# Performance work log

Hardware: AMD Instinct MI355X
Metric: run time of the kernel (lower is better)

The kernel has to match this reference:

```python
import jax, jax.numpy as jnp
import numpy as np

# Module config (from init_kwargs): causal=False, window_size=(256,256), window_type=0,
# softmax_scale=None -> 1/sqrt(D), dropout=0 (eval mode).
WINDOW_LEFT, WINDOW_RIGHT = 256, 256


def _window_mask(Sq, Sk, causal, use_window_mask):
    """Boolean [Sq, Sk] visibility mask, FA2 semantics (right-aligned offset)."""
    qi = jnp.arange(Sq)[:, None]
    kj = jnp.arange(Sk)[None, :]
    offset = Sk - Sq
    if causal:
        return kj <= qi + offset  # window (-1, 0)
    if use_window_mask:
        m = jnp.ones((Sq, Sk), dtype=bool)
        if WINDOW_LEFT >= 0:
            m = m & (kj >= qi + offset - WINDOW_LEFT)
        if WINDOW_RIGHT >= 0:
            m = m & (kj <= qi + offset + WINDOW_RIGHT)
        return m
    return None  # full attention


def setup_inputs() -> dict:
    key = jax.random.key(0)
    kq, kkv = jax.random.split(key)
    B, Sq, Sk, H, D = 2, 2048, 2048, 16, 64
    q = jax.random.normal(kq, (B, Sq, H, D), dtype=jnp.float32)
    kv = jax.random.normal(kkv, (B, Sk, 2, H, D), dtype=jnp.float32)
    return {"q": q, "kv": kv, "causal": 0, "use_window_mask": 1, "return_attn_probs": 0}


def reference(q, kv, causal, use_window_mask, return_attn_probs):
    # q: (B, Sq, H, D); kv: (B, Sk, 2, H, D)
    B, Sq, H, D = q.shape
    Sk = kv.shape[1]
    k = kv[:, :, 0]  # (B, Sk, H, D)
    v = kv[:, :, 1]
    scale = 1.0 / (D ** 0.5)
    scores = jnp.einsum('bqhd,bkhd->bhqk', q, k) * scale  # (B, H, Sq, Sk)
    mask = _window_mask(Sq, Sk, bool(causal), bool(use_window_mask))
    if mask is not None:
        scores = jnp.where(mask[None, None], scores, jnp.finfo(scores.dtype).min)
    probs = jax.nn.softmax(scores, axis=-1)
    out = jnp.einsum('bhqk,bkhd->bqhd', probs, v)  # (B, Sq, H, D)
    return out
```

## Files before the change

### kernel.cpp

```cpp
#include <hip/hip_runtime.h>
#include <hip/hip_bf16.h>

#define B_    2
#define SQ_   2048
#define SK_   2048
#define NH_   16
#define DH_   64
#define WIN_  256
#define NEG_  -30000.0f

typedef __bf16 bf16_t;
typedef bf16_t bf16x8 __attribute__((ext_vector_type(8)));
typedef bf16_t bf16x4 __attribute__((ext_vector_type(4)));
typedef float  f32x4  __attribute__((ext_vector_type(4)));

#define KSTRIDE 72
#define VSTRIDE 40
#define PSTRIDE 40

__global__ __launch_bounds__(256, 2)
void fa_fwd(const float* __restrict__ qg, const float* __restrict__ kvg,
            float* __restrict__ outg) {
  const int tid  = threadIdx.x;
  const int wid  = tid >> 6;
  const int lane = tid & 63;
  const int quad = lane >> 4;
  const int li   = lane & 15;

  const int bid = blockIdx.x;
  const int qb  = bid & 31;
  const int bh  = bid >> 5;
  const int b   = bh >> 4;
  const int h   = bh & 15;

  const int q0b = qb * 64;
  const int q0  = q0b + wid * 16;

  __shared__ __align__(16) bf16_t sK [32 * KSTRIDE];
  __shared__ __align__(16) bf16_t sVT[64 * VSTRIDE];
  __shared__ __align__(16) bf16_t sP [4 * 16 * PSTRIDE];
  bf16_t* pl = sP + wid * 16 * PSTRIDE;

  const float qscale = 0.125f * 1.44269504088896340736f;
  const float* qrow = qg + ((size_t)((b * SQ_ + q0 + li) * NH_ + h)) * DH_;
  bf16x8 qfrag[2];
#pragma unroll
  for (int c = 0; c < 2; ++c) {
    f32x4 a0 = *(const f32x4*)(qrow + c * 32 + quad * 8);
    f32x4 a1 = *(const f32x4*)(qrow + c * 32 + quad * 8 + 4);
#pragma unroll
    for (int i = 0; i < 4; ++i) {
      qfrag[c][i]     = (bf16_t)(a0[i] * qscale);
      qfrag[c][i + 4] = (bf16_t)(a1[i] * qscale);
    }
  }

  f32x4 oacc[4];
#pragma unroll
  for (int t = 0; t < 4; ++t) { f32x4 z = {0.f, 0.f, 0.f, 0.f}; oacc[t] = z; }
  float m = NEG_, l = 0.f;

  int klo = q0b - WIN_; if (klo < 0) klo = 0; klo &= ~31;
  int khi = q0b + 63 + WIN_ + 1; if (khi > SK_) khi = SK_; khi = (khi + 31) & ~31;

  const float* kbase = kvg + (size_t)b * SK_ * 2 * NH_ * DH_ + (size_t)h * DH_;
  const float* vbase = kbase + NH_ * DH_;
  const size_t krow_stride = 2 * NH_ * DH_;

  const int skey = tid >> 3;
  const int sd0  = (tid & 7) * 8;

  for (int kk = klo; kk < khi; kk += 32) {
    {
      const float* kr = kbase + (size_t)(kk + skey) * krow_stride + sd0;
      f32x4 a0 = *(const f32x4*)kr;
      f32x4 a1 = *(const f32x4*)(kr + 4);
      bf16x8 w;
#pragma unroll
      for (int i = 0; i < 4; ++i) { w[i] = (bf16_t)a0[i]; w[i + 4] = (bf16_t)a1[i]; }
      *(bf16x8*)(sK + skey * KSTRIDE + sd0) = w;

      const float* vr = vbase + (size_t)(kk + skey) * krow_stride + sd0;
      f32x4 b0 = *(const f32x4*)vr;
      f32x4 b1 = *(const f32x4*)(vr + 4);
#pragma unroll
      for (int i = 0; i < 4; ++i) {
        sVT[(sd0 + i)     * VSTRIDE + skey] = (bf16_t)b0[i];
        sVT[(sd0 + 4 + i) * VSTRIDE + skey] = (bf16_t)b1[i];
      }
    }
    __syncthreads();

    f32x4 sc[2];
#pragma unroll
    for (int s = 0; s < 2; ++s) {
      bf16x8 kf0 = *(const bf16x8*)(sK + (s * 16 + li) * KSTRIDE + quad * 8);
      bf16x8 kf1 = *(const bf16x8*)(sK + (s * 16 + li) * KSTRIDE + 32 + quad * 8);
      f32x4 acc = {0.f, 0.f, 0.f, 0.f};
      acc = __builtin_amdgcn_mfma_f32_16x16x32_bf16(kf0, qfrag[0], acc, 0, 0, 0);
      acc = __builtin_amdgcn_mfma_f32_16x16x32_bf16(kf1, qfrag[1], acc, 0, 0, 0);
      sc[s] = acc;
    }

    const int qa = q0 + li;
#pragma unroll
    for (int s = 0; s < 2; ++s)
#pragma unroll
      for (int r = 0; r < 4; ++r) {
        int key = kk + s * 16 + quad * 4 + r;
        unsigned dd = (unsigned)(key - qa + WIN_);
        if (dd > 2u * WIN_) sc[s][r] = NEG_;
      }

    float tmax = fmaxf(fmaxf(fmaxf(sc[0][0], sc[0][1]), fmaxf(sc[0][2], sc[0][3])),
                       fmaxf(fmaxf(sc[1][0], sc[1][1]), fmaxf(sc[1][2], sc[1][3])));
    tmax = fmaxf(tmax, __shfl_xor(tmax, 16));
    tmax = fmaxf(tmax, __shfl_xor(tmax, 32));
    float mnew  = fmaxf(m, tmax);
    float alpha = exp2f(m - mnew);
    float psum = 0.f;
    bf16x4 pk[2];
#pragma unroll
    for (int s = 0; s < 2; ++s)
#pragma unroll
      for (int r = 0; r < 4; ++r) {
        float p = exp2f(sc[s][r] - mnew);
        psum += p;
        pk[s][r] = (bf16_t)p;
      }
    psum += __shfl_xor(psum, 16);
    psum += __shfl_xor(psum, 32);
    l = l * alpha + psum;
    m = mnew;

#pragma unroll
    for (int s = 0; s < 2; ++s)
      *(bf16x4*)(pl + li * PSTRIDE + s * 16 + quad * 4) = pk[s];

    __syncthreads();

    float al[4];
#pragma unroll
    for (int r = 0; r < 4; ++r) al[r] = __shfl(alpha, quad * 4 + r);
#pragma unroll
    for (int t = 0; t < 4; ++t) {
      oacc[t][0] *= al[0]; oacc[t][1] *= al[1];
      oacc[t][2] *= al[2]; oacc[t][3] *= al[3];
    }

    bf16x8 pf = *(const bf16x8*)(pl + li * PSTRIDE + quad * 8);
#pragma unroll
    for (int t = 0; t < 4; ++t) {
      bf16x8 vf = *(const bf16x8*)(sVT + (16 * t + li) * VSTRIDE + quad * 8);
      oacc[t] = __builtin_amdgcn_mfma_f32_16x16x32_bf16(pf, vf, oacc[t], 0, 0, 0);
    }
    __syncthreads();
  }

  float rl[4];
#pragma unroll
  for (int r = 0; r < 4; ++r) {
    float lv = __shfl(l, quad * 4 + r);
    rl[r] = 1.0f / lv;
  }
  float* orow = outg + ((size_t)((b * SQ_ + q0) * NH_ + h)) * DH_;
#pragma unroll
  for (int t = 0; t < 4; ++t)
#pragma unroll
    for (int r = 0; r < 4; ++r)
      orow[(size_t)(quad * 4 + r) * (NH_ * DH_) + 16 * t + li] = oacc[t][r] * rl[r];
}

extern "C" void kernel_launch(void* const* d_in, const int* in_sizes, int n_in,
                              void* d_out, int out_size, void* d_ws, size_t ws_size,
                              hipStream_t stream) {
  (void)in_sizes; (void)n_in; (void)out_size; (void)d_ws; (void)ws_size;
  const float* q  = (const float*)d_in[0];
  const float* kv = (const float*)d_in[1];
  float* out = (float*)d_out;
  dim3 grid(B_ * NH_ * (SQ_ / 64));
  fa_fwd<<<grid, 256, 0, stream>>>(q, kv, out);
}
```

Before: 133.8 us.

## Enlarge query and key tiles, prefetch KV into registers, drop mid-iteration barrier

Each block now handles 128 queries, with each wave owning two 16-row query tiles, and processes 64 keys per step, so every K/V tile staged in shared memory is reused by twice as many queries. The next K/V chunk is loaded into registers while the current chunk is computed, and the barrier between writing P and reading it is replaced with an LDS waitcnt, since each wave only reads its own P rows. Block indexing is reordered so that heads vary fastest. The cost is higher register pressure and fewer blocks (512 instead of 1024), which may reduce occupancy and the number of waves available to hide latency.

```diff
diff --git a/kernel.cpp b/kernel.cpp
--- a/kernel.cpp
+++ b/kernel.cpp
@@ -15,8 +15,8 @@
 typedef float  f32x4  __attribute__((ext_vector_type(4)));
 
 #define KSTRIDE 72
-#define VSTRIDE 40
-#define PSTRIDE 40
+#define VSTRIDE 72
+#define PSTRIDE 72
 
 __global__ __launch_bounds__(256, 2)
 void fa_fwd(const float* __restrict__ qg, const float* __restrict__ kvg,
@@ -28,147 +28,182 @@
   const int li   = lane & 15;
 
   const int bid = blockIdx.x;
-  const int qb  = bid & 31;
-  const int bh  = bid >> 5;
+  const int qb  = bid >> 5;
+  const int bh  = bid & 31;
   const int b   = bh >> 4;
   const int h   = bh & 15;
 
-  const int q0b = qb * 64;
-  const int q0  = q0b + wid * 16;
-
-  __shared__ __align__(16) bf16_t sK [32 * KSTRIDE];
+  const int q0b = qb * 128;
+  const int q0  = q0b + wid * 32;
+
+  __shared__ __align__(16) bf16_t sK [64 * KSTRIDE];
   __shared__ __align__(16) bf16_t sVT[64 * VSTRIDE];
-  __shared__ __align__(16) bf16_t sP [4 * 16 * PSTRIDE];
-  bf16_t* pl = sP + wid * 16 * PSTRIDE;
+  __shared__ __align__(16) bf16_t sP [4 * 32 * PSTRIDE];
+  bf16_t* pl = sP + wid * 32 * PSTRIDE;
 
   const float qscale = 0.125f * 1.44269504088896340736f;
-  const float* qrow = qg + ((size_t)((b * SQ_ + q0 + li) * NH_ + h)) * DH_;
-  bf16x8 qfrag[2];
-#pragma unroll
-  for (int c = 0; c < 2; ++c) {
-    f32x4 a0 = *(const f32x4*)(qrow + c * 32 + quad * 8);
-    f32x4 a1 = *(const f32x4*)(qrow + c * 32 + quad * 8 + 4);
-#pragma unroll
-    for (int i = 0; i < 4; ++i) {
-      qfrag[c][i]     = (bf16_t)(a0[i] * qscale);
-      qfrag[c][i + 4] = (bf16_t)(a1[i] * qscale);
-    }
-  }
-
-  f32x4 oacc[4];
-#pragma unroll
-  for (int t = 0; t < 4; ++t) { f32x4 z = {0.f, 0.f, 0.f, 0.f}; oacc[t] = z; }
-  float m = NEG_, l = 0.f;
-
-  int klo = q0b - WIN_; if (klo < 0) klo = 0; klo &= ~31;
-  int khi = q0b + 63 + WIN_ + 1; if (khi > SK_) khi = SK_; khi = (khi + 31) & ~31;
+  bf16x8 qfrag[2][2];
+#pragma unroll
+  for (int qt = 0; qt < 2; ++qt) {
+    const float* qrow = qg + ((size_t)((b * SQ_ + q0 + qt * 16 + li) * NH_ + h)) * DH_;
+#pragma unroll
+    for (int c = 0; c < 2; ++c) {
+      f32x4 a0 = *(const f32x4*)(qrow + c * 32 + quad * 8);
+      f32x4 a1 = *(const f32x4*)(qrow + c * 32 + quad * 8 + 4);
+#pragma unroll
+      for (int i = 0; i < 4; ++i) {
+        qfrag[qt][c][i]     = (bf16_t)(a0[i] * qscale);
+        qfrag[qt][c][i + 4] = (bf16_t)(a1[i] * qscale);
+      }
+    }
+  }
+
+  f32x4 oacc[2][4];
+#pragma unroll
+  for (int qt = 0; qt < 2; ++qt)
+#pragma unroll
+    for (int t = 0; t < 4; ++t) { f32x4 z = {0.f, 0.f, 0.f, 0.f}; oacc[qt][t] = z; }
+  float m[2] = {NEG_, NEG_}, l[2] = {0.f, 0.f};
+
+  int klo = q0b - WIN_; if (klo < 0) klo = 0;
+  int khi = q0b + 127 + WIN_ + 1; if (khi > SK_) khi = SK_;
 
   const float* kbase = kvg + (size_t)b * SK_ * 2 * NH_ * DH_ + (size_t)h * DH_;
   const float* vbase = kbase + NH_ * DH_;
   const size_t krow_stride = 2 * NH_ * DH_;
 
-  const int skey = tid >> 3;
-  const int sd0  = (tid & 7) * 8;
-
-  for (int kk = klo; kk < khi; kk += 32) {
+  const int skey = tid >> 2;
+  const int sd0  = (tid & 3) * 16;
+
+  f32x4 ka[4], va[4];
+  {
+    const float* kr = kbase + (size_t)(klo + skey) * krow_stride + sd0;
+    const float* vr = vbase + (size_t)(klo + skey) * krow_stride + sd0;
+#pragma unroll
+    for (int i = 0; i < 4; ++i) { ka[i] = *(const f32x4*)(kr + 4 * i); va[i] = *(const f32x4*)(vr + 4 * i); }
+  }
+
+  for (int kk = klo; kk < khi; kk += 64) {
     {
-      const float* kr = kbase + (size_t)(kk + skey) * krow_stride + sd0;
-      f32x4 a0 = *(const f32x4*)kr;
-      f32x4 a1 = *(const f32x4*)(kr + 4);
-      bf16x8 w;
-#pragma unroll
-      for (int i = 0; i < 4; ++i) { w[i] = (bf16_t)a0[i]; w[i + 4] = (bf16_t)a1[i]; }
-      *(bf16x8*)(sK + skey * KSTRIDE + sd0) = w;
-
-      const float* vr = vbase + (size_t)(kk + skey) * krow_stride + sd0;
-      f32x4 b0 = *(const f32x4*)vr;
-      f32x4 b1 = *(const f32x4*)(vr + 4);
+      bf16x8 w0, w1;
 #pragma unroll
       for (int i = 0; i < 4; ++i) {
-        sVT[(sd0 + i)     * VSTRIDE + skey] = (bf16_t)b0[i];
-        sVT[(sd0 + 4 + i) * VSTRIDE + skey] = (bf16_t)b1[i];
-      }
+        w0[i] = (bf16_t)ka[0][i]; w0[i + 4] = (bf16_t)ka[1][i];
+        w1[i] = (bf16_t)ka[2][i]; w1[i + 4] = (bf16_t)ka[3][i];
+      }
+      *(bf16x8*)(sK + skey * KSTRIDE + sd0)     = w0;
+      *(bf16x8*)(sK + skey * KSTRIDE + sd0 + 8) = w1;
+#pragma unroll
+      for (int i = 0; i < 4; ++i)
+#pragma unroll
+        for (int j = 0; j < 4; ++j)
+          sVT[(sd0 + 4 * i + j) * VSTRIDE + skey] = (bf16_t)va[i][j];
     }
     __syncthreads();
 
-    f32x4 sc[2];
-#pragma unroll
-    for (int s = 0; s < 2; ++s) {
+    if (kk + 64 < khi) {
+      const float* kr = kbase + (size_t)(kk + 64 + skey) * krow_stride + sd0;
+      const float* vr = vbase + (size_t)(kk + 64 + skey) * krow_stride + sd0;
+#pragma unroll
+      for (int i = 0; i < 4; ++i) { ka[i] = *(const f32x4*)(kr + 4 * i); va[i] = *(const f32x4*)(vr + 4 * i); }
+    }
+
+    f32x4 sc[2][4];
+#pragma unroll
+    for (int s = 0; s < 4; ++s) {
       bf16x8 kf0 = *(const bf16x8*)(sK + (s * 16 + li) * KSTRIDE + quad * 8);
       bf16x8 kf1 = *(const bf16x8*)(sK + (s * 16 + li) * KSTRIDE + 32 + quad * 8);
-      f32x4 acc = {0.f, 0.f, 0.f, 0.f};
-      acc = __builtin_amdgcn_mfma_f32_16x16x32_bf16(kf0, qfrag[0], acc, 0, 0, 0);
-      acc = __builtin_amdgcn_mfma_f32_16x16x32_bf16(kf1, qfrag[1], acc, 0, 0, 0);
-      sc[s] = acc;
-    }
-
-    const int qa = q0 + li;
-#pragma unroll
-    for (int s = 0; s < 2; ++s)
-#pragma unroll
-      for (int r = 0; r < 4; ++r) {
-        int key = kk + s * 16 + quad * 4 + r;
-        unsigned dd = (unsigned)(key - qa + WIN_);
-        if (dd > 2u * WIN_) sc[s][r] = NEG_;
-      }
-
-    float tmax = fmaxf(fmaxf(fmaxf(sc[0][0], sc[0][1]), fmaxf(sc[0][2], sc[0][3])),
-                       fmaxf(fmaxf(sc[1][0], sc[1][1]), fmaxf(sc[1][2], sc[1][3])));
-    tmax = fmaxf(tmax, __shfl_xor(tmax, 16));
-    tmax = fmaxf(tmax, __shfl_xor(tmax, 32));
-    float mnew  = fmaxf(m, tmax);
-    float alpha = exp2f(m - mnew);
-    float psum = 0.f;
-    bf16x4 pk[2];
-#pragma unroll
-    for (int s = 0; s < 2; ++s)
-#pragma unroll
-      for (int r = 0; r < 4; ++r) {
-        float p = exp2f(sc[s][r] - mnew);
-        psum += p;
-        pk[s][r] = (bf16_t)p;
-      }
-    psum += __shfl_xor(psum, 16);
-    psum += __shfl_xor(psum, 32);
-    l = l * alpha + psum;
-    m = mnew;
-
-#pragma unroll
-    for (int s = 0; s < 2; ++s)
-      *(bf16x4*)(pl + li * PSTRIDE + s * 16 + quad * 4) = pk[s];
-
+#pragma unroll
+      for (int qt = 0; qt < 2; ++qt) {
+        f32x4 acc = {0.f, 0.f, 0.f, 0.f};
+        acc = __builtin_amdgcn_mfma_f32_16x16x32_bf16(kf0, qfrag[qt][0], acc, 0, 0, 0);
+        acc = __builtin_amdgcn_mfma_f32_16x16x32_bf16(kf1, qfrag[qt][1], acc, 0, 0, 0);
+        sc[qt][s] = acc;
+      }
+    }
+
+    float alpha[2];
+#pragma unroll
+    for (int qt = 0; qt < 2; ++qt) {
+      const int qa = q0 + qt * 16 + li;
+#pragma unroll
+      for (int s = 0; s < 4; ++s)
+#pragma unroll
+        for (int r = 0; r < 4; ++r) {
+          int key = kk + s * 16 + quad * 4 + r;
+          unsigned dd = (unsigned)(key - qa + WIN_);
+          if (dd > 2u * WIN_) sc[qt][s][r] = NEG_;
+        }
+      float tmax = NEG_;
+#pragma unroll
+      for (int s = 0; s < 4; ++s)
+        tmax = fmaxf(tmax, fmaxf(fmaxf(sc[qt][s][0], sc[qt][s][1]),
+                                 fmaxf(sc[qt][s][2], sc[qt][s][3])));
+      tmax = fmaxf(tmax, __shfl_xor(tmax, 16));
+      tmax = fmaxf(tmax, __shfl_xor(tmax, 32));
+      float mnew = fmaxf(m[qt], tmax);
+      alpha[qt] = exp2f(m[qt] - mnew);
+      float psum = 0.f;
+#pragma unroll
+      for (int s = 0; s < 4; ++s) {
+        bf16x4 pk;
+#pragma unroll
+        for (int r = 0; r < 4; ++r) {
+          float p = exp2f(sc[qt][s][r] - mnew);
+          psum += p;
+          pk[r] = (bf16_t)p;
+        }
+        *(bf16x4*)(pl + (qt * 16 + li) * PSTRIDE + s * 16 + quad * 4) = pk;
+      }
+      psum += __shfl_xor(psum, 16);
+      psum += __shfl_xor(psum, 32);
+      l[qt] = l[qt] * alpha[qt] + psum;
+      m[qt] = mnew;
+    }
+
+    asm volatile("s_waitcnt lgkmcnt(0)" ::: "memory");
+
+#pragma unroll
+    for (int qt = 0; qt < 2; ++qt) {
+      float al[4];
+#pragma unroll
+      for (int r = 0; r < 4; ++r) al[r] = __shfl(alpha[qt], quad * 4 + r);
+#pragma unroll
+      for (int t = 0; t < 4; ++t) {
+        oacc[qt][t][0] *= al[0]; oacc[qt][t][1] *= al[1];
+        oacc[qt][t][2] *= al[2]; oacc[qt][t][3] *= al[3];
+      }
+    }
+
+#pragma unroll
+    for (int kc = 0; kc < 2; ++kc) {
+      bf16x8 pf0 = *(const bf16x8*)(pl + li * PSTRIDE + kc * 32 + quad * 8);
+      bf16x8 pf1 = *(const bf16x8*)(pl + (16 + li) * PSTRIDE + kc * 32 + quad * 8);
+#pragma unroll
+      for (int t = 0; t < 4; ++t) {
+        bf16x8 vf = *(const bf16x8*)(sVT + (16 * t + li) * VSTRIDE + kc * 32 + quad * 8);
+        oacc[0][t] = __builtin_amdgcn_mfma_f32_16x16x32_bf16(pf0, vf, oacc[0][t], 0, 0, 0);
+        oacc[1][t] = __builtin_amdgcn_mfma_f32_16x16x32_bf16(pf1, vf, oacc[1][t], 0, 0, 0);
+      }
+    }
     __syncthreads();
-
-    float al[4];
-#pragma unroll
-    for (int r = 0; r < 4; ++r) al[r] = __shfl(alpha, quad * 4 + r);
-#pragma unroll
-    for (int t = 0; t < 4; ++t) {
-      oacc[t][0] *= al[0]; oacc[t][1] *= al[1];
-      oacc[t][2] *= al[2]; oacc[t][3] *= al[3];
-    }
-
-    bf16x8 pf = *(const bf16x8*)(pl + li * PSTRIDE + quad * 8);
-#pragma unroll
-    for (int t = 0; t < 4; ++t) {
-      bf16x8 vf = *(const bf16x8*)(sVT + (16 * t + li) * VSTRIDE + quad * 8);
-      oacc[t] = __builtin_amdgcn_mfma_f32_16x16x32_bf16(pf, vf, oacc[t], 0, 0, 0);
-    }
-    __syncthreads();
-  }
-
-  float rl[4];
-#pragma unroll
-  for (int r = 0; r < 4; ++r) {
-    float lv = __shfl(l, quad * 4 + r);
-    rl[r] = 1.0f / lv;
-  }
-  float* orow = outg + ((size_t)((b * SQ_ + q0) * NH_ + h)) * DH_;
-#pragma unroll
-  for (int t = 0; t < 4; ++t)
-#pragma unroll
-    for (int r = 0; r < 4; ++r)
-      orow[(size_t)(quad * 4 + r) * (NH_ * DH_) + 16 * t + li] = oacc[t][r] * rl[r];
+  }
+
+#pragma unroll
+  for (int qt = 0; qt < 2; ++qt) {
+    float rl[4];
+#pragma unroll
+    for (int r = 0; r < 4; ++r) {
+      float lv = __shfl(l[qt], quad * 4 + r);
+      rl[r] = 1.0f / lv;
+    }
+    float* orow = outg + ((size_t)((b * SQ_ + q0 + qt * 16) * NH_ + h)) * DH_;
+#pragma unroll
+    for (int t = 0; t < 4; ++t)
+#pragma unroll
+      for (int r = 0; r < 4; ++r)
+        orow[(size_t)(quad * 4 + r) * (NH_ * DH_) + 16 * t + li] = oacc[qt][t][r] * rl[r];
+  }
 }
 
 extern "C" void kernel_launch(void* const* d_in, const int* in_sizes, int n_in,
@@ -178,6 +213,6 @@
   const float* q  = (const float*)d_in[0];
   const float* kv = (const float*)d_in[1];
   float* out = (float*)d_out;
-  dim3 grid(B_ * NH_ * (SQ_ / 64));
+  dim3 grid(B_ * NH_ * (SQ_ / 128));
   fa_fwd<<<grid, 256, 0, stream>>>(q, kv, out);
 }
```

Result: faster. 119.3 us (-10.9%).

## Double-buffer K/V tiles with register prefetch, 128-query blocks, per-warp window skipping

Applied to the files above, without the earlier changes.

Each block now handles 128 queries with 512 threads and steps through 64-key tiles. The K/V shared-memory tiles are double-buffered: the next tile's global loads are issued into registers before computing on the current tile, which removes one barrier per iteration. Warps skip tiles that fall outside their own 16-query window and apply mask arithmetic only on edge tiles. The transposed V layout gets an XOR swizzle to reduce LDS bank conflicts. The grid index order is changed so adjacent blocks share a query block across heads. The costs are more shared memory, higher register pressure, and the risk that the launch bound of 4 blocks of 512 threads cannot be met.

```diff
diff --git a/kernel.cpp b/kernel.cpp
--- a/kernel.cpp
+++ b/kernel.cpp
@@ -15,10 +15,10 @@
 typedef float  f32x4  __attribute__((ext_vector_type(4)));
 
 #define KSTRIDE 72
-#define VSTRIDE 40
-#define PSTRIDE 40
-
-__global__ __launch_bounds__(256, 2)
+#define VSTRIDE 72
+#define PSTRIDE 72
+
+__global__ __launch_bounds__(512, 4)
 void fa_fwd(const float* __restrict__ qg, const float* __restrict__ kvg,
             float* __restrict__ outg) {
   const int tid  = threadIdx.x;
@@ -28,18 +28,18 @@
   const int li   = lane & 15;
 
   const int bid = blockIdx.x;
-  const int qb  = bid & 31;
-  const int bh  = bid >> 5;
+  const int qb  = bid >> 5;
+  const int bh  = bid & 31;
   const int b   = bh >> 4;
   const int h   = bh & 15;
 
-  const int q0b = qb * 64;
+  const int q0b = qb * 128;
   const int q0  = q0b + wid * 16;
 
-  __shared__ __align__(16) bf16_t sK [32 * KSTRIDE];
-  __shared__ __align__(16) bf16_t sVT[64 * VSTRIDE];
-  __shared__ __align__(16) bf16_t sP [4 * 16 * PSTRIDE];
-  bf16_t* pl = sP + wid * 16 * PSTRIDE;
+  __shared__ __align__(16) bf16_t sK [2][64 * KSTRIDE];
+  __shared__ __align__(16) bf16_t sVT[2][64 * VSTRIDE];
+  __shared__ __align__(16) bf16_t sP [8][16 * PSTRIDE];
+  bf16_t* pl = sP[wid];
 
   const float qscale = 0.125f * 1.44269504088896340736f;
   const float* qrow = qg + ((size_t)((b * SQ_ + q0 + li) * NH_ + h)) * DH_;
@@ -60,8 +60,8 @@
   for (int t = 0; t < 4; ++t) { f32x4 z = {0.f, 0.f, 0.f, 0.f}; oacc[t] = z; }
   float m = NEG_, l = 0.f;
 
-  int klo = q0b - WIN_; if (klo < 0) klo = 0; klo &= ~31;
-  int khi = q0b + 63 + WIN_ + 1; if (khi > SK_) khi = SK_; khi = (khi + 31) & ~31;
+  int klo = q0b - WIN_; if (klo < 0) klo = 0;
+  int khi = q0b + 127 + WIN_ + 1; if (khi > SK_) khi = SK_;
 
   const float* kbase = kvg + (size_t)b * SK_ * 2 * NH_ * DH_ + (size_t)h * DH_;
   const float* vbase = kbase + NH_ * DH_;
@@ -69,92 +69,121 @@
 
   const int skey = tid >> 3;
   const int sd0  = (tid & 7) * 8;
-
-  for (int kk = klo; kk < khi; kk += 32) {
-    {
-      const float* kr = kbase + (size_t)(kk + skey) * krow_stride + sd0;
-      f32x4 a0 = *(const f32x4*)kr;
-      f32x4 a1 = *(const f32x4*)(kr + 4);
+  const int vcol = skey ^ (((sd0 >> 3) & 7) << 3);
+
+  f32x4 ka[2], va[2];
+  {
+    const float* kr = kbase + (size_t)(klo + skey) * krow_stride + sd0;
+    const float* vr = vbase + (size_t)(klo + skey) * krow_stride + sd0;
+    ka[0] = *(const f32x4*)kr;       ka[1] = *(const f32x4*)(kr + 4);
+    va[0] = *(const f32x4*)vr;       va[1] = *(const f32x4*)(vr + 4);
+  }
+  {
+    bf16x8 w;
+#pragma unroll
+    for (int i = 0; i < 4; ++i) { w[i] = (bf16_t)ka[0][i]; w[i + 4] = (bf16_t)ka[1][i]; }
+    *(bf16x8*)(&sK[0][skey * KSTRIDE + sd0]) = w;
+#pragma unroll
+    for (int i = 0; i < 4; ++i) {
+      sVT[0][(sd0 + i)     * VSTRIDE + vcol] = (bf16_t)va[0][i];
+      sVT[0][(sd0 + 4 + i) * VSTRIDE + vcol] = (bf16_t)va[1][i];
+    }
+  }
+  __syncthreads();
+
+  int buf = 0;
+  for (int kk = klo; kk < khi; kk += 64) {
+    const bool nxt = (kk + 64 < khi);
+    if (nxt) {
+      const float* kr = kbase + (size_t)(kk + 64 + skey) * krow_stride + sd0;
+      const float* vr = vbase + (size_t)(kk + 64 + skey) * krow_stride + sd0;
+      ka[0] = *(const f32x4*)kr;       ka[1] = *(const f32x4*)(kr + 4);
+      va[0] = *(const f32x4*)vr;       va[1] = *(const f32x4*)(vr + 4);
+    }
+
+    if (kk + 63 >= q0 - WIN_ && kk <= q0 + 15 + WIN_) {
+      f32x4 sc[4];
+#pragma unroll
+      for (int s = 0; s < 4; ++s) {
+        bf16x8 kf0 = *(const bf16x8*)(&sK[buf][(s * 16 + li) * KSTRIDE + quad * 8]);
+        bf16x8 kf1 = *(const bf16x8*)(&sK[buf][(s * 16 + li) * KSTRIDE + 32 + quad * 8]);
+        f32x4 acc = {0.f, 0.f, 0.f, 0.f};
+        acc = __builtin_amdgcn_mfma_f32_16x16x32_bf16(kf0, qfrag[0], acc, 0, 0, 0);
+        acc = __builtin_amdgcn_mfma_f32_16x16x32_bf16(kf1, qfrag[1], acc, 0, 0, 0);
+        sc[s] = acc;
+      }
+      if (kk < q0 - 241 || kk > q0 + 193) {
+        const int qa = q0 + li;
+#pragma unroll
+        for (int s = 0; s < 4; ++s)
+#pragma unroll
+          for (int r = 0; r < 4; ++r) {
+            int key = kk + s * 16 + quad * 4 + r;
+            unsigned dd = (unsigned)(key - qa + WIN_);
+            if (dd > 2u * WIN_) sc[s][r] = NEG_;
+          }
+      }
+      float tmax = NEG_;
+#pragma unroll
+      for (int s = 0; s < 4; ++s)
+        tmax = fmaxf(tmax, fmaxf(fmaxf(sc[s][0], sc[s][1]), fmaxf(sc[s][2], sc[s][3])));
+      tmax = fmaxf(tmax, __shfl_xor(tmax, 16));
+      tmax = fmaxf(tmax, __shfl_xor(tmax, 32));
+      float mnew  = fmaxf(m, tmax);
+      float alpha = exp2f(m - mnew);
+      float psum = 0.f;
+#pragma unroll
+      for (int s = 0; s < 4; ++s) {
+        bf16x4 pk;
+#pragma unroll
+        for (int r = 0; r < 4; ++r) {
+          float p = exp2f(sc[s][r] - mnew);
+          psum += p;
+          pk[r] = (bf16_t)p;
+        }
+        *(bf16x4*)(&pl[li * PSTRIDE + s * 16 + quad * 4]) = pk;
+      }
+      psum += __shfl_xor(psum, 16);
+      psum += __shfl_xor(psum, 32);
+      l = l * alpha + psum;
+      m = mnew;
+
+      asm volatile("s_waitcnt lgkmcnt(0)" ::: "memory");
+
+      float al[4];
+#pragma unroll
+      for (int r = 0; r < 4; ++r) al[r] = __shfl(alpha, quad * 4 + r);
+#pragma unroll
+      for (int t = 0; t < 4; ++t) {
+        oacc[t][0] *= al[0]; oacc[t][1] *= al[1];
+        oacc[t][2] *= al[2]; oacc[t][3] *= al[3];
+      }
+#pragma unroll
+      for (int kc = 0; kc < 2; ++kc) {
+        bf16x8 pf = *(const bf16x8*)(&pl[li * PSTRIDE + kc * 32 + quad * 8]);
+#pragma unroll
+        for (int t = 0; t < 4; ++t) {
+          const int d = 16 * t + li;
+          const int c = ((2 * t + (li >> 3)) & 7) << 3;
+          bf16x8 vf = *(const bf16x8*)(&sVT[buf][d * VSTRIDE + ((kc * 32 + quad * 8) ^ c)]);
+          oacc[t] = __builtin_amdgcn_mfma_f32_16x16x32_bf16(pf, vf, oacc[t], 0, 0, 0);
+        }
+      }
+    }
+
+    if (nxt) {
       bf16x8 w;
 #pragma unroll
-      for (int i = 0; i < 4; ++i) { w[i] = (bf16_t)a0[i]; w[i + 4] = (bf16_t)a1[i]; }
-      *(bf16x8*)(sK + skey * KSTRIDE + sd0) = w;
-
-      const float* vr = vbase + (size_t)(kk + skey) * krow_stride + sd0;
-      f32x4 b0 = *(const f32x4*)vr;
-      f32x4 b1 = *(const f32x4*)(vr + 4);
+      for (int i = 0; i < 4; ++i) { w[i] = (bf16_t)ka[0][i]; w[i + 4] = (bf16_t)ka[1][i]; }
+      *(bf16x8*)(&sK[buf ^ 1][skey * KSTRIDE + sd0]) = w;
 #pragma unroll
       for (int i = 0; i < 4; ++i) {
-        sVT[(sd0 + i)     * VSTRIDE + skey] = (bf16_t)b0[i];
-        sVT[(sd0 + 4 + i) * VSTRIDE + skey] = (bf16_t)b1[i];
+        sVT[buf ^ 1][(sd0 + i)     * VSTRIDE + vcol] = (bf16_t)va[0][i];
+        sVT[buf ^ 1][(sd0 + 4 + i) * VSTRIDE + vcol] = (bf16_t)va[1][i];
       }
     }
     __syncthreads();
-
-    f32x4 sc[2];
-#pragma unroll
-    for (int s = 0; s < 2; ++s) {
-      bf16x8 kf0 = *(const bf16x8*)(sK + (s * 16 + li) * KSTRIDE + quad * 8);
-      bf16x8 kf1 = *(const bf16x8*)(sK + (s * 16 + li) * KSTRIDE + 32 + quad * 8);
-      f32x4 acc = {0.f, 0.f, 0.f, 0.f};
-      acc = __builtin_amdgcn_mfma_f32_16x16x32_bf16(kf0, qfrag[0], acc, 0, 0, 0);
-      acc = __builtin_amdgcn_mfma_f32_16x16x32_bf16(kf1, qfrag[1], acc, 0, 0, 0);
-      sc[s] = acc;
-    }
-
-    const int qa = q0 + li;
-#pragma unroll
-    for (int s = 0; s < 2; ++s)
-#pragma unroll
-      for (int r = 0; r < 4; ++r) {
-        int key = kk + s * 16 + quad * 4 + r;
-        unsigned dd = (unsigned)(key - qa + WIN_);
-        if (dd > 2u * WIN_) sc[s][r] = NEG_;
-      }
-
-    float tmax = fmaxf(fmaxf(fmaxf(sc[0][0], sc[0][1]), fmaxf(sc[0][2], sc[0][3])),
-                       fmaxf(fmaxf(sc[1][0], sc[1][1]), fmaxf(sc[1][2], sc[1][3])));
-    tmax = fmaxf(tmax, __shfl_xor(tmax, 16));
-    tmax = fmaxf(tmax, __shfl_xor(tmax, 32));
-    float mnew  = fmaxf(m, tmax);
-    float alpha = exp2f(m - mnew);
-    float psum = 0.f;
-    bf16x4 pk[2];
-#pragma unroll
-    for (int s = 0; s < 2; ++s)
-#pragma unroll
-      for (int r = 0; r < 4; ++r) {
-        float p = exp2f(sc[s][r] - mnew);
-        psum += p;
-        pk[s][r] = (bf16_t)p;
-      }
-    psum += __shfl_xor(psum, 16);
-    psum += __shfl_xor(psum, 32);
-    l = l * alpha + psum;
-    m = mnew;
-
-#pragma unroll
-    for (int s = 0; s < 2; ++s)
-      *(bf16x4*)(pl + li * PSTRIDE + s * 16 + quad * 4) = pk[s];
-
-    __syncthreads();
-
-    float al[4];
-#pragma unroll
-    for (int r = 0; r < 4; ++r) al[r] = __shfl(alpha, quad * 4 + r);
-#pragma unroll
-    for (int t = 0; t < 4; ++t) {
-      oacc[t][0] *= al[0]; oacc[t][1] *= al[1];
-      oacc[t][2] *= al[2]; oacc[t][3] *= al[3];
-    }
-
-    bf16x8 pf = *(const bf16x8*)(pl + li * PSTRIDE + quad * 8);
-#pragma unroll
-    for (int t = 0; t < 4; ++t) {
-      bf16x8 vf = *(const bf16x8*)(sVT + (16 * t + li) * VSTRIDE + quad * 8);
-      oacc[t] = __builtin_amdgcn_mfma_f32_16x16x32_bf16(pf, vf, oacc[t], 0, 0, 0);
-    }
-    __syncthreads();
+    buf ^= 1;
   }
 
   float rl[4];
@@ -178,6 +207,6 @@
   const float* q  = (const float*)d_in[0];
   const float* kv = (const float*)d_in[1];
   float* out = (float*)d_out;
-  dim3 grid(B_ * NH_ * (SQ_ / 64));
-  fa_fwd<<<grid, 256, 0, stream>>>(q, kv, out);
+  dim3 grid(B_ * NH_ * (SQ_ / 128));
+  fa_fwd<<<grid, 512, 0, stream>>>(q, kv, out);
 }
```

Result: faster. 111.9 us (-16.4%).
